# Kernel tuning notes

Measured on AMD Instinct MI355X. Metric: run time of the kernel, lower is better.

Reference implementation:

```python
import jax, jax.numpy as jnp
import numpy as np

T = 2048         # seq_len (nbatch in original code)
IN = 384         # input_size (npts)
H = 2 * IN       # hidden_dim = 768
NL = 10          # n_layers
NOUT = 384       # output_size


def setup_inputs() -> dict:
    key = jax.random.key(0)
    ks = jax.random.split(key, 12)
    s_in = 1.0 / np.sqrt(H)  # PyTorch GRU init scale
    inp = {
        "x": jax.random.normal(ks[0], (T, IN), dtype=jnp.float32),
        # layer 0 (input_size -> H)
        "w_ih0": jax.random.uniform(ks[1], (3 * H, IN), jnp.float32, -s_in, s_in),
        "w_hh0": jax.random.uniform(ks[2], (3 * H, H), jnp.float32, -s_in, s_in),
        "b_ih0": jax.random.uniform(ks[3], (3 * H,), jnp.float32, -s_in, s_in),
        "b_hh0": jax.random.uniform(ks[4], (3 * H,), jnp.float32, -s_in, s_in),
        # layers 1..9 (H -> H), stacked
        "w_ih": jax.random.uniform(ks[5], (NL - 1, 3 * H, H), jnp.float32, -s_in, s_in),
        "w_hh": jax.random.uniform(ks[6], (NL - 1, 3 * H, H), jnp.float32, -s_in, s_in),
        "b_ih": jax.random.uniform(ks[7], (NL - 1, 3 * H), jnp.float32, -s_in, s_in),
        "b_hh": jax.random.uniform(ks[8], (NL - 1, 3 * H), jnp.float32, -s_in, s_in),
        # final linear head
        "fc_w": jax.random.uniform(ks[9], (NOUT, H), jnp.float32, -s_in, s_in),
        "fc_b": jax.random.uniform(ks[10], (NOUT,), jnp.float32, -s_in, s_in),
    }
    return inp


def _gru_layer(xs, w_ih, w_hh, b_ih, b_hh):
    # xs: [T, D_in] -> ys: [T, H]. PyTorch GRU cell semantics.
    gi = xs @ w_ih.T + b_ih          # [T, 3H] input projections, batched GEMM up front

    def step(h, gi_t):
        gh = h @ w_hh.T + b_hh       # [3H]
        i_r, i_z, i_n = jnp.split(gi_t, 3)
        h_r, h_z, h_n = jnp.split(gh, 3)
        r = jax.nn.sigmoid(i_r + h_r)
        z = jax.nn.sigmoid(i_z + h_z)
        n = jnp.tanh(i_n + r * h_n)
        h_new = (1.0 - z) * n + z * h
        return h_new, h_new

    h0 = jnp.zeros((xs.shape[1] if False else w_hh.shape[1],), xs.dtype)  # [H]
    _, ys = jax.lax.scan(step, h0, gi)
    return ys


def reference(x, w_ih0, w_hh0, b_ih0, b_hh0, w_ih, w_hh, b_ih, b_hh, fc_w, fc_b):
    # batch_size = 1 in the original; hidden initialized to zeros each call.
    h = _gru_layer(x, w_ih0, w_hh0, b_ih0, b_hh0)   # layer 0
    for l in range(NL - 1):                           # layers 1..9 (fixed small loop)
        h = _gru_layer(h, w_ih[l], w_hh[l], b_ih[l], b_hh[l])
    out = h @ fc_w.T + fc_b                           # [T, NOUT]
    return out
```

## Files before the change

### kernel.cpp

```cpp
#include <hip/hip_runtime.h>


#define T_SEQ 2048
#define H_DIM 768
#define IN0   384
#define G3    2304
#define NLAYER 10
#define BPL   24
#define NBLK  (NLAYER * BPL)
#define UPB   32
#define NTHR  512
#define NOUT  384
#define CTR_STRIDE 32
#define RING  16
#define WPR   384
#define WIH_STRIDE 776
#define HCS_STRIDE 52
#define HSD_STRIDE 56
#define HSD0_STRIDE 32

typedef _Float16 half2_t __attribute__((ext_vector_type(2)));
typedef _Float16 half8_t __attribute__((ext_vector_type(8)));
typedef unsigned long long u64;

__device__ __forceinline__ float sigm(float x) { return 1.0f / (1.0f + __expf(-x)); }

__device__ __forceinline__ u64 ld64(const u64* p) {
    return __hip_atomic_load(p, __ATOMIC_RELAXED, __HIP_MEMORY_SCOPE_AGENT);
}
__device__ __forceinline__ void st64(u64* p, u64 v) {
    __hip_atomic_store(p, v, __ATOMIC_RELAXED, __HIP_MEMORY_SCOPE_AGENT);
}
__device__ __forceinline__ unsigned ldctr(const unsigned* p) {
    return __hip_atomic_load(p, __ATOMIC_RELAXED, __HIP_MEMORY_SCOPE_AGENT);
}
__device__ __forceinline__ int tagok(u64 v, unsigned tg) {
    return (((unsigned)v & 31u) == tg) & ((((unsigned)(v >> 32)) & 31u) == tg);
}

__device__ __forceinline__ float dot8(half8_t h, half8_t w, float acc) {
    union U { half8_t v; unsigned u[4]; };
    U H; H.v = h; U W; W.v = w;
#pragma unroll
    for (int j = 0; j < 4; ++j) {
#if __has_builtin(__builtin_amdgcn_fdot2)
        acc = __builtin_amdgcn_fdot2(__builtin_bit_cast(half2_t, H.u[j]),
                                     __builtin_bit_cast(half2_t, W.u[j]), acc, false);
#else
        half2_t a = __builtin_bit_cast(half2_t, H.u[j]);
        half2_t b = __builtin_bit_cast(half2_t, W.u[j]);
        asm volatile("v_dot2_f32_f16 %0, %1, %2, %0" : "+v"(acc) : "v"(a), "v"(b));
#endif
    }
    return acc;
}

extern "C" __global__ __launch_bounds__(NTHR, 1) void gru_flow(
    const float* __restrict__ x,
    const float* __restrict__ wih0,
    const float* __restrict__ whh0,
    const float* __restrict__ bih0,
    const float* __restrict__ bhh0,
    const float* __restrict__ wihS,
    const float* __restrict__ whhS,
    const float* __restrict__ bihS,
    const float* __restrict__ bhhS,
    u64* __restrict__ ring64,
    float* __restrict__ h9,
    unsigned int* __restrict__ ctr)
{
    __shared__ __align__(16) _Float16 wih16[96 * WIH_STRIDE];
    __shared__ __align__(16) float    hcs[2][16 * HCS_STRIDE];
    __shared__ __align__(16) _Float16 hsd16[2][16 * HSD_STRIDE];

    const int tid  = threadIdx.x;
    const int lane = tid & 63;
    const int wv   = tid >> 6;
    const int p    = lane & 15;
    const int ulocal = wv * 4 + (lane >> 4);
    const int bid  = blockIdx.x;
    const int layer = bid / BPL;
    const int sub   = bid % BPL;
    const int uglob = sub * UPB + ulocal;
    const int Din   = layer ? H_DIM : IN0;

    const float* wihL = layer ? wihS + (size_t)(layer - 1) * G3 * H_DIM : wih0;
    const float* whhL = layer ? whhS + (size_t)(layer - 1) * G3 * H_DIM : whh0;
    const float* bihL = layer ? bihS + (size_t)(layer - 1) * G3 : bih0;
    const float* bhhL = layer ? bhhS + (size_t)(layer - 1) * G3 : bhh0;

    float4 wr[3][12];
#pragma unroll
    for (int gate = 0; gate < 3; ++gate) {
        const float4* src = (const float4*)(whhL + (size_t)(uglob + gate * H_DIM) * H_DIM + 48 * p);
#pragma unroll
        for (int i = 0; i < 12; ++i) wr[gate][i] = src[i];
    }
    const float bhr  = bhhL[uglob], bhz = bhhL[uglob + H_DIM], bhn  = bhhL[uglob + 2 * H_DIM];
    const float bir  = bihL[uglob], biz = bihL[uglob + H_DIM], bin_ = bihL[uglob + 2 * H_DIM];

    for (int rr = 0; rr < 12; ++rr) {
        const int r = wv * 12 + rr;
        const int u = r / 3, G = r % 3;
        const float* src = wihL + (size_t)(sub * UPB + u + G * H_DIM) * Din;
        _Float16* dst = wih16 + r * WIH_STRIDE;
        for (int k = lane; k < Din; k += 64) dst[k] = (_Float16)src[k];
    }
    __syncthreads();

    auto stage_hsd = [&](int b, int w, u64 v) {
        const int s = w / 24, idx = (2 * w) % 48;
        const _Float16 a = (_Float16)__uint_as_float((unsigned)v & ~31u);
        const _Float16 c = (_Float16)__uint_as_float((unsigned)(v >> 32) & ~31u);
        const unsigned pk = (unsigned)__builtin_bit_cast(unsigned short, a)
                          | ((unsigned)__builtin_bit_cast(unsigned short, c) << 16);
        *(unsigned*)&hsd16[b][s * HSD_STRIDE + idx] = pk;
    };

    float gi_r = 0.f, gi_z = 0.f, gi_n = 0.f;
    auto ih_gemv = [&](int b) {
        float sr = 0.f, sz = 0.f, sn = 0.f;
        if (layer) {
            const half8_t* h8 = (const half8_t*)(&hsd16[b][p * HSD_STRIDE]);
            const half8_t* w0 = (const half8_t*)(wih16 + (ulocal * 3 + 0) * WIH_STRIDE + 48 * p);
            const half8_t* w1 = (const half8_t*)(wih16 + (ulocal * 3 + 1) * WIH_STRIDE + 48 * p);
            const half8_t* wn = (const half8_t*)(wih16 + (ulocal * 3 + 2) * WIH_STRIDE + 48 * p);
#pragma unroll
            for (int i = 0; i < 6; ++i) {
                const half8_t hv = h8[i];
                sr = dot8(hv, w0[i], sr);
                sz = dot8(hv, w1[i], sz);
                sn = dot8(hv, wn[i], sn);
            }
        } else {
            const half8_t* h8 = (const half8_t*)(&hsd16[b][p * HSD0_STRIDE]);
            const half8_t* w0 = (const half8_t*)(wih16 + (ulocal * 3 + 0) * WIH_STRIDE + 24 * p);
            const half8_t* w1 = (const half8_t*)(wih16 + (ulocal * 3 + 1) * WIH_STRIDE + 24 * p);
            const half8_t* wn = (const half8_t*)(wih16 + (ulocal * 3 + 2) * WIH_STRIDE + 24 * p);
#pragma unroll
            for (int i = 0; i < 3; ++i) {
                const half8_t hv = h8[i];
                sr = dot8(hv, w0[i], sr);
                sz = dot8(hv, w1[i], sz);
                sn = dot8(hv, wn[i], sn);
            }
        }
#pragma unroll
        for (int off = 1; off <= 8; off <<= 1) {
            sr += __shfl_xor(sr, off, 64);
            sz += __shfl_xor(sz, off, 64);
            sn += __shfl_xor(sn, off, 64);
        }
        gi_r = sr + bir; gi_z = sz + biz; gi_n = sn + bin_;
    };

    if (layer) {
        if (tid < WPR) {
            const u64* sp = ring64 + (size_t)(layer - 1) * RING * WPR;
            u64 v = 0;
            while (!tagok(v, 1u)) v = ld64(sp + tid);
            stage_hsd(1, tid, v);
        }
    } else {
        if (tid < IN0) hsd16[1][(tid / 24) * HSD0_STRIDE + tid % 24] = (_Float16)x[tid];
    }
    __syncthreads();
    ih_gemv(1);

    u64 ca0 = 0, sa0 = 0;
    float xs = 0.f;
    if (tid < WPR) {
        if (layer) sa0 = ld64(ring64 + ((size_t)(layer - 1) * RING + 1) * WPR + tid);
        else       xs  = x[IN0 + tid];
    }

    unsigned bp = 0;

    for (int t = 0; t < T_SEQ; ++t) {
        const int b = t & 1;
        const bool have_s = (t + 1) < T_SEQ;

        if (layer != NLAYER - 1 && t >= 16 && (t & 3) == 0) {
            const unsigned tgt = 24u * (unsigned)((t - 12) >> 2);
            while (bp < tgt) {
                __builtin_amdgcn_s_sleep(2);
                bp = ldctr(&ctr[(layer + 1) * CTR_STRIDE]);
            }
        }

        if (t > 0 && tid < WPR) {
            const u64* hr = ring64 + ((size_t)layer * RING + ((t - 1) & (RING - 1))) * WPR;
            const unsigned tg = (unsigned)t & 31u;
            u64 v = ca0;
            while (!tagok(v, tg)) v = ld64(hr + tid);
            const int s = tid / 24, idx = (2 * tid) % 48;
            float2 hv;
            hv.x = __uint_as_float((unsigned)v & ~31u);
            hv.y = __uint_as_float((unsigned)(v >> 32) & ~31u);
            *(float2*)&hcs[b][s * HCS_STRIDE + idx] = hv;
        }

        if (have_s) {
            if (layer) {
                if (tid < WPR) {
                    const u64* sp = ring64 + ((size_t)(layer - 1) * RING + ((t + 1) & (RING - 1))) * WPR;
                    const unsigned tg2 = (unsigned)(t + 2) & 31u;
                    u64 v = sa0;
                    while (!tagok(v, tg2)) v = ld64(sp + tid);
                    stage_hsd(b, tid, v);
                }
            } else {
                if (tid < IN0) hsd16[b][(tid / 24) * HSD0_STRIDE + tid % 24] = (_Float16)xs;
            }
        }

        __syncthreads();

        float ar = 0.f, az = 0.f, an = 0.f;
        if (t > 0) {
            const float4* hs = (const float4*)(&hcs[b][p * HCS_STRIDE]);
#pragma unroll
            for (int i = 0; i < 12; ++i) {
                const float4 h4 = hs[i];
                ar += h4.x * wr[0][i].x + h4.y * wr[0][i].y + h4.z * wr[0][i].z + h4.w * wr[0][i].w;
                az += h4.x * wr[1][i].x + h4.y * wr[1][i].y + h4.z * wr[1][i].z + h4.w * wr[1][i].w;
                an += h4.x * wr[2][i].x + h4.y * wr[2][i].y + h4.z * wr[2][i].z + h4.w * wr[2][i].w;
            }
        }
#pragma unroll
        for (int off = 1; off <= 8; off <<= 1) {
            ar += __shfl_xor(ar, off, 64);
            az += __shfl_xor(az, off, 64);
            an += __shfl_xor(an, off, 64);
        }
        {
            const float hp = (t > 0) ? hcs[b][(uglob / 48) * HCS_STRIDE + uglob % 48] : 0.f;
            const float r = sigm(ar + bhr + gi_r);
            const float z = sigm(az + bhz + gi_z);
            const float n = tanhf(gi_n + r * (an + bhn));
            const float hnew = (1.f - z) * n + z * hp;
            const float hpart = __shfl_xor(hnew, 16, 64);
            if (p == 0 && (lane & 16) == 0) {
                const unsigned tg1 = (unsigned)(t + 1) & 31u;
                const unsigned lo = (__float_as_uint(hnew)  & ~31u) | tg1;
                const unsigned hi = (__float_as_uint(hpart) & ~31u) | tg1;
                st64(&ring64[((size_t)layer * RING + (t & (RING - 1))) * WPR + (uglob >> 1)],
                     ((u64)hi << 32) | (u64)lo);
            }
            if (layer == NLAYER - 1 && p == 0) h9[(size_t)t * H_DIM + uglob] = hnew;
        }

        if (have_s && tid < WPR) {
            ca0 = ld64(ring64 + ((size_t)layer * RING + (t & (RING - 1))) * WPR + tid);
            if ((t + 2) < T_SEQ) {
                if (layer) sa0 = ld64(ring64 + ((size_t)(layer - 1) * RING + ((t + 2) & (RING - 1))) * WPR + tid);
                else       xs  = x[(size_t)(t + 2) * IN0 + tid];
            }
        }

        if (have_s) ih_gemv(b);

        if ((t & 3) == 3) {
            if (tid == 0 && layer)
                __hip_atomic_fetch_add(&ctr[layer * CTR_STRIDE], 1u,
                                       __ATOMIC_RELAXED, __HIP_MEMORY_SCOPE_AGENT);
            if (layer != NLAYER - 1)
                bp = ldctr(&ctr[(layer + 1) * CTR_STRIDE]);
        }
    }
}

extern "C" __global__ __launch_bounds__(NOUT, 1) void fc_head(
    const float* __restrict__ h,
    const float* __restrict__ fw,
    const float* __restrict__ fb,
    float* __restrict__ out)
{
    __shared__ float hs[H_DIM];
    const int t = blockIdx.x;
    const float* hr = h + (size_t)t * H_DIM;
    for (int k = threadIdx.x; k < H_DIM; k += NOUT) hs[k] = hr[k];
    __syncthreads();

    const int o = threadIdx.x;
    const float4* wr4 = (const float4*)(fw + (size_t)o * H_DIM);
    const float4* hs4 = (const float4*)hs;
    float acc = fb[o];
#pragma unroll 8
    for (int k = 0; k < H_DIM / 4; ++k) {
        const float4 w = wr4[k], hv = hs4[k];
        acc += w.x * hv.x + w.y * hv.y + w.z * hv.z + w.w * hv.w;
    }
    out[(size_t)t * NOUT + o] = acc;
}

extern "C" void kernel_launch(void* const* d_in, const int* in_sizes, int n_in,
                              void* d_out, int out_size, void* d_ws, size_t ws_size,
                              hipStream_t stream)
{
    const float* x    = (const float*)d_in[0];
    const float* wih0 = (const float*)d_in[1];
    const float* whh0 = (const float*)d_in[2];
    const float* bih0 = (const float*)d_in[3];
    const float* bhh0 = (const float*)d_in[4];
    const float* wihS = (const float*)d_in[5];
    const float* whhS = (const float*)d_in[6];
    const float* bihS = (const float*)d_in[7];
    const float* bhhS = (const float*)d_in[8];
    const float* fcw  = (const float*)d_in[9];
    const float* fcb  = (const float*)d_in[10];

    char* ws = (char*)d_ws;
    unsigned int* ctr = (unsigned int*)ws;
    u64* ring64 = (u64*)(ws + 65536);
    float* h9   = (float*)(ws + 65536 + (size_t)NLAYER * RING * WPR * 8);

    hipMemsetAsync(ctr, 0, 65536, stream);
    hipMemsetAsync(ring64, 0, (size_t)NLAYER * RING * WPR * 8, stream);

    hipLaunchKernelGGL(gru_flow, dim3(NBLK), dim3(NTHR), 0, stream,
                       x, wih0, whh0, bih0, bhh0, wihS, whhS, bihS, bhhS,
                       ring64, h9, ctr);

    hipLaunchKernelGGL(fc_head, dim3(T_SEQ), dim3(NOUT), 0, stream,
                       h9, fcw, fcb, (float*)d_out);
}
```

Measured before the change: 7.046 ms.

## Split GRU stack into two 5-layer phases with XCD-local role assignment

Instead of one persistent kernel running all 10 layers as a dataflow pipeline, the work is split into two launches of 5 layers each, joined by an fp16 intermediate buffer. Each block reads its XCD id and claims a layer role on that XCD, so all blocks of a layer sit on one XCD and can exchange the recurrent hidden state through near-scope (sc0) loads and stores. A second ring carries state downstream to the next layer over agent scope. The goal is lower latency on the per-step recurrent sync. In exchange the pipeline fill is paid twice, role claiming adds spin waits at startup, and results depend on how the hardware places blocks on XCDs.

```diff
diff --git a/kernel.cpp b/kernel.cpp
--- a/kernel.cpp
+++ b/kernel.cpp
@@ -5,9 +5,10 @@
 #define H_DIM 768
 #define IN0   384
 #define G3    2304
-#define NLAYER 10
+#define NLL   5
 #define BPL   24
-#define NBLK  (NLAYER * BPL)
+#define NROLE (NLL * BPL)
+#define NBLK  256
 #define UPB   32
 #define NTHR  512
 #define NOUT  384
@@ -25,11 +26,20 @@
 
 __device__ __forceinline__ float sigm(float x) { return 1.0f / (1.0f + __expf(-x)); }
 
-__device__ __forceinline__ u64 ld64(const u64* p) {
+__device__ __forceinline__ u64 ld64_far(const u64* p) {
     return __hip_atomic_load(p, __ATOMIC_RELAXED, __HIP_MEMORY_SCOPE_AGENT);
 }
-__device__ __forceinline__ void st64(u64* p, u64 v) {
+__device__ __forceinline__ void st64_far(u64* p, u64 v) {
     __hip_atomic_store(p, v, __ATOMIC_RELAXED, __HIP_MEMORY_SCOPE_AGENT);
+}
+__device__ __forceinline__ u64 ld64_near(const u64* p) {
+    u64 v;
+    asm volatile("global_load_dwordx2 %0, %1, off sc0\n\ts_waitcnt vmcnt(0)"
+                 : "=v"(v) : "v"(p) : "memory");
+    return v;
+}
+__device__ __forceinline__ void st64_near(u64* p, u64 v) {
+    asm volatile("global_store_dwordx2 %0, %1, off sc0" :: "v"(p), "v"(v) : "memory");
 }
 __device__ __forceinline__ unsigned ldctr(const unsigned* p) {
     return __hip_atomic_load(p, __ATOMIC_RELAXED, __HIP_MEMORY_SCOPE_AGENT);
@@ -55,39 +65,74 @@
     return acc;
 }
 
-extern "C" __global__ __launch_bounds__(NTHR, 1) void gru_flow(
-    const float* __restrict__ x,
-    const float* __restrict__ wih0,
-    const float* __restrict__ whh0,
-    const float* __restrict__ bih0,
-    const float* __restrict__ bhh0,
-    const float* __restrict__ wihS,
-    const float* __restrict__ whhS,
-    const float* __restrict__ bihS,
-    const float* __restrict__ bhhS,
-    u64* __restrict__ ring64,
-    float* __restrict__ h9,
-    unsigned int* __restrict__ ctr)
+extern "C" __global__ __launch_bounds__(NTHR, 1) void gru_phase(
+    const void* fin, int fin_is16, int layer_base,
+    const float* __restrict__ wih0, const float* __restrict__ whh0,
+    const float* __restrict__ bih0, const float* __restrict__ bhh0,
+    const float* __restrict__ wihS, const float* __restrict__ whhS,
+    const float* __restrict__ bihS, const float* __restrict__ bhhS,
+    u64* __restrict__ ring_loc, u64* __restrict__ ring_dwn,
+    unsigned int* __restrict__ ctr, int* __restrict__ taken,
+    int* __restrict__ rolexcd,
+    float* __restrict__ hout32, _Float16* __restrict__ hout16)
 {
     __shared__ __align__(16) _Float16 wih16[96 * WIH_STRIDE];
     __shared__ __align__(16) float    hcs[2][16 * HCS_STRIDE];
     __shared__ __align__(16) _Float16 hsd16[2][16 * HSD_STRIDE];
+    __shared__ int s_role, s_local;
 
     const int tid  = threadIdx.x;
     const int lane = tid & 63;
     const int wv   = tid >> 6;
     const int p    = lane & 15;
     const int ulocal = wv * 4 + (lane >> 4);
-    const int bid  = blockIdx.x;
-    const int layer = bid / BPL;
-    const int sub   = bid % BPL;
+
+    if (tid == 0) {
+        int xcd = 0;
+        asm volatile("s_getreg_b32 %0, hwreg(20, 0, 32)" : "=s"(xcd));
+        xcd &= 7;
+        int role = -1;
+        if (xcd < NLL) {
+            const int b0 = xcd * BPL;
+            for (int r = b0; r < b0 + BPL; ++r)
+                if (atomicExch(&taken[r], 1) == 0) { role = r; break; }
+        }
+        if (role < 0) {
+            for (int w = 0; w < 300; ++w) __builtin_amdgcn_s_sleep(8);
+            for (int r = 0; r < NROLE && role < 0; ++r)
+                if (atomicExch(&taken[r], 1) == 0) role = r;
+        }
+        int loc = 0;
+        if (role >= 0) {
+            __hip_atomic_store(&rolexcd[role], xcd + 1,
+                               __ATOMIC_RELEASE, __HIP_MEMORY_SCOPE_AGENT);
+            const int lb = (role / BPL) * BPL;
+            loc = 1;
+            for (int r = lb; r < lb + BPL; ++r) {
+                int v;
+                while ((v = __hip_atomic_load(&rolexcd[r], __ATOMIC_ACQUIRE,
+                                              __HIP_MEMORY_SCOPE_AGENT)) == 0)
+                    __builtin_amdgcn_s_sleep(2);
+                if (v != xcd + 1) loc = 0;
+            }
+        }
+        s_role = role; s_local = loc;
+    }
+    __syncthreads();
+    const int role = s_role;
+    if (role < 0) return;
+    const bool uselocal = (s_local != 0);
+    const int layer = role / BPL;
+    const int sub   = role % BPL;
     const int uglob = sub * UPB + ulocal;
-    const int Din   = layer ? H_DIM : IN0;
-
-    const float* wihL = layer ? wihS + (size_t)(layer - 1) * G3 * H_DIM : wih0;
-    const float* whhL = layer ? whhS + (size_t)(layer - 1) * G3 * H_DIM : whh0;
-    const float* bihL = layer ? bihS + (size_t)(layer - 1) * G3 : bih0;
-    const float* bhhL = layer ? bhhS + (size_t)(layer - 1) * G3 : bhh0;
+    const int lg    = layer_base + layer;
+    const int Din   = lg ? H_DIM : IN0;
+    const bool din384 = (Din == IN0);
+
+    const float* wihL = lg ? wihS + (size_t)(lg - 1) * G3 * H_DIM : wih0;
+    const float* whhL = lg ? whhS + (size_t)(lg - 1) * G3 * H_DIM : whh0;
+    const float* bihL = lg ? bihS + (size_t)(lg - 1) * G3 : bih0;
+    const float* bhhL = lg ? bhhS + (size_t)(lg - 1) * G3 : bhh0;
 
     float4 wr[3][12];
 #pragma unroll
@@ -116,11 +161,23 @@
                           | ((unsigned)__builtin_bit_cast(unsigned short, c) << 16);
         *(unsigned*)&hsd16[b][s * HSD_STRIDE + idx] = pk;
     };
+    auto stage_fin = [&](int b, int row) {
+        if (din384) {
+            if (tid < IN0)
+                hsd16[b][(tid / 24) * HSD0_STRIDE + tid % 24] = fin_is16
+                    ? ((const _Float16*)fin)[(size_t)row * IN0 + tid]
+                    : (_Float16)((const float*)fin)[(size_t)row * IN0 + tid];
+        } else {
+            const _Float16* f16 = (const _Float16*)fin;
+            for (int vi = tid; vi < H_DIM; vi += NTHR)
+                hsd16[b][(vi / 48) * HSD_STRIDE + vi % 48] = f16[(size_t)row * H_DIM + vi];
+        }
+    };
 
     float gi_r = 0.f, gi_z = 0.f, gi_n = 0.f;
     auto ih_gemv = [&](int b) {
         float sr = 0.f, sz = 0.f, sn = 0.f;
-        if (layer) {
+        if (!din384) {
             const half8_t* h8 = (const half8_t*)(&hsd16[b][p * HSD_STRIDE]);
             const half8_t* w0 = (const half8_t*)(wih16 + (ulocal * 3 + 0) * WIH_STRIDE + 48 * p);
             const half8_t* w1 = (const half8_t*)(wih16 + (ulocal * 3 + 1) * WIH_STRIDE + 48 * p);
@@ -128,9 +185,7 @@
 #pragma unroll
             for (int i = 0; i < 6; ++i) {
                 const half8_t hv = h8[i];
-                sr = dot8(hv, w0[i], sr);
-                sz = dot8(hv, w1[i], sz);
-                sn = dot8(hv, wn[i], sn);
+                sr = dot8(hv, w0[i], sr); sz = dot8(hv, w1[i], sz); sn = dot8(hv, wn[i], sn);
             }
         } else {
             const half8_t* h8 = (const half8_t*)(&hsd16[b][p * HSD0_STRIDE]);
@@ -140,9 +195,7 @@
 #pragma unroll
             for (int i = 0; i < 3; ++i) {
                 const half8_t hv = h8[i];
-                sr = dot8(hv, w0[i], sr);
-                sz = dot8(hv, w1[i], sz);
-                sn = dot8(hv, wn[i], sn);
+                sr = dot8(hv, w0[i], sr); sz = dot8(hv, w1[i], sz); sn = dot8(hv, wn[i], sn);
             }
         }
 #pragma unroll
@@ -156,23 +209,20 @@
 
     if (layer) {
         if (tid < WPR) {
-            const u64* sp = ring64 + (size_t)(layer - 1) * RING * WPR;
+            const u64* sp = ring_dwn + (size_t)(layer - 1) * RING * WPR + tid;
             u64 v = 0;
-            while (!tagok(v, 1u)) v = ld64(sp + tid);
+            while (!tagok(v, 1u)) v = ld64_far(sp);
             stage_hsd(1, tid, v);
         }
     } else {
-        if (tid < IN0) hsd16[1][(tid / 24) * HSD0_STRIDE + tid % 24] = (_Float16)x[tid];
+        stage_fin(1, 0);
     }
     __syncthreads();
     ih_gemv(1);
 
-    u64 ca0 = 0, sa0 = 0;
-    float xs = 0.f;
-    if (tid < WPR) {
-        if (layer) sa0 = ld64(ring64 + ((size_t)(layer - 1) * RING + 1) * WPR + tid);
-        else       xs  = x[IN0 + tid];
-    }
+    u64 sa0 = 0;
+    if (layer && tid < WPR)
+        sa0 = ld64_far(ring_dwn + ((size_t)(layer - 1) * RING + 1) * WPR + tid);
 
     unsigned bp = 0;
 
@@ -180,7 +230,7 @@
         const int b = t & 1;
         const bool have_s = (t + 1) < T_SEQ;
 
-        if (layer != NLAYER - 1 && t >= 16 && (t & 3) == 0) {
+        if (layer != NLL - 1 && t >= 16 && (t & 3) == 0) {
             const unsigned tgt = 24u * (unsigned)((t - 12) >> 2);
             while (bp < tgt) {
                 __builtin_amdgcn_s_sleep(2);
@@ -189,10 +239,11 @@
         }
 
         if (t > 0 && tid < WPR) {
-            const u64* hr = ring64 + ((size_t)layer * RING + ((t - 1) & (RING - 1))) * WPR;
+            const u64* hr = ring_loc + ((size_t)layer * RING + ((t - 1) & (RING - 1))) * WPR + tid;
             const unsigned tg = (unsigned)t & 31u;
-            u64 v = ca0;
-            while (!tagok(v, tg)) v = ld64(hr + tid);
+            u64 v = ld64_near(hr);
+            int k = 0;
+            while (!tagok(v, tg)) v = (++k & 1) ? ld64_far(hr) : ld64_near(hr);
             const int s = tid / 24, idx = (2 * tid) % 48;
             float2 hv;
             hv.x = __uint_as_float((unsigned)v & ~31u);
@@ -203,14 +254,14 @@
         if (have_s) {
             if (layer) {
                 if (tid < WPR) {
-                    const u64* sp = ring64 + ((size_t)(layer - 1) * RING + ((t + 1) & (RING - 1))) * WPR;
+                    const u64* sp = ring_dwn + ((size_t)(layer - 1) * RING + ((t + 1) & (RING - 1))) * WPR + tid;
                     const unsigned tg2 = (unsigned)(t + 2) & 31u;
                     u64 v = sa0;
-                    while (!tagok(v, tg2)) v = ld64(sp + tid);
+                    while (!tagok(v, tg2)) v = ld64_far(sp);
                     stage_hsd(b, tid, v);
                 }
             } else {
-                if (tid < IN0) hsd16[b][(tid / 24) * HSD0_STRIDE + tid % 24] = (_Float16)xs;
+                stage_fin(b, t + 1);
             }
         }
 
@@ -244,19 +295,20 @@
                 const unsigned tg1 = (unsigned)(t + 1) & 31u;
                 const unsigned lo = (__float_as_uint(hnew)  & ~31u) | tg1;
                 const unsigned hi = (__float_as_uint(hpart) & ~31u) | tg1;
-                st64(&ring64[((size_t)layer * RING + (t & (RING - 1))) * WPR + (uglob >> 1)],
-                     ((u64)hi << 32) | (u64)lo);
-            }
-            if (layer == NLAYER - 1 && p == 0) h9[(size_t)t * H_DIM + uglob] = hnew;
-        }
-
-        if (have_s && tid < WPR) {
-            ca0 = ld64(ring64 + ((size_t)layer * RING + (t & (RING - 1))) * WPR + tid);
-            if ((t + 2) < T_SEQ) {
-                if (layer) sa0 = ld64(ring64 + ((size_t)(layer - 1) * RING + ((t + 2) & (RING - 1))) * WPR + tid);
-                else       xs  = x[(size_t)(t + 2) * IN0 + tid];
-            }
-        }
+                const u64 w = ((u64)hi << 32) | (u64)lo;
+                const size_t base = ((size_t)layer * RING + (t & (RING - 1))) * WPR + (uglob >> 1);
+                if (uselocal) st64_near(&ring_loc[base], w);
+                else          st64_far (&ring_loc[base], w);
+                if (layer < NLL - 1) st64_far(&ring_dwn[base], w);
+            }
+            if (layer == NLL - 1 && p == 0) {
+                if (hout16) hout16[(size_t)t * H_DIM + uglob] = (_Float16)hnew;
+                else        hout32[(size_t)t * H_DIM + uglob] = hnew;
+            }
+        }
+
+        if (layer && tid < WPR && (t + 2) < T_SEQ)
+            sa0 = ld64_far(ring_dwn + ((size_t)(layer - 1) * RING + ((t + 2) & (RING - 1))) * WPR + tid);
 
         if (have_s) ih_gemv(b);
 
@@ -264,7 +316,7 @@
             if (tid == 0 && layer)
                 __hip_atomic_fetch_add(&ctr[layer * CTR_STRIDE], 1u,
                                        __ATOMIC_RELAXED, __HIP_MEMORY_SCOPE_AGENT);
-            if (layer != NLAYER - 1)
+            if (layer != NLL - 1)
                 bp = ldctr(&ctr[(layer + 1) * CTR_STRIDE]);
         }
     }
@@ -311,16 +363,34 @@
     const float* fcb  = (const float*)d_in[10];
 
     char* ws = (char*)d_ws;
-    unsigned int* ctr = (unsigned int*)ws;
-    u64* ring64 = (u64*)(ws + 65536);
-    float* h9   = (float*)(ws + 65536 + (size_t)NLAYER * RING * WPR * 8);
-
-    hipMemsetAsync(ctr, 0, 65536, stream);
-    hipMemsetAsync(ring64, 0, (size_t)NLAYER * RING * WPR * 8, stream);
-
-    hipLaunchKernelGGL(gru_flow, dim3(NBLK), dim3(NTHR), 0, stream,
-                       x, wih0, whh0, bih0, bhh0, wihS, whhS, bihS, bhhS,
-                       ring64, h9, ctr);
+    const size_t RSZ = (size_t)NLL * RING * WPR * 8;
+    int*      taken0   = (int*)(ws + 0);
+    int*      taken1   = (int*)(ws + 1024);
+    int*      rolexcd0 = (int*)(ws + 2048);
+    int*      rolexcd1 = (int*)(ws + 3072);
+    unsigned* ctr0     = (unsigned*)(ws + 8192);
+    unsigned* ctr1     = (unsigned*)(ws + 16384);
+    u64* ring_loc0 = (u64*)(ws + 65536);
+    u64* ring_dwn0 = (u64*)(ws + 65536 + RSZ);
+    u64* ring_loc1 = (u64*)(ws + 65536 + 2 * RSZ);
+    u64* ring_dwn1 = (u64*)(ws + 65536 + 3 * RSZ);
+    _Float16* h4 = (_Float16*)(ws + 1048576);
+    float*    h9 = (float*)(ws + 4194304);
+
+    hipMemsetAsync(ws, 0, 65536, stream);
+    hipMemsetAsync(ws + 65536, 0, 4 * RSZ, stream);
+
+    hipLaunchKernelGGL(gru_phase, dim3(NBLK), dim3(NTHR), 0, stream,
+                       (const void*)x, 0, 0,
+                       wih0, whh0, bih0, bhh0, wihS, whhS, bihS, bhhS,
+                       ring_loc0, ring_dwn0, ctr0, taken0, rolexcd0,
+                       (float*)nullptr, h4);
+
+    hipLaunchKernelGGL(gru_phase, dim3(NBLK), dim3(NTHR), 0, stream,
+                       (const void*)h4, 1, NLL,
+                       wih0, whh0, bih0, bhh0, wihS, whhS, bihS, bhhS,
+                       ring_loc1, ring_dwn1, ctr1, taken1, rolexcd1,
+                       h9, (_Float16*)nullptr);
 
     hipLaunchKernelGGL(fc_head, dim3(T_SEQ), dim3(NOUT), 0, stream,
                        h9, fcw, fcb, (float*)d_out);
```

After: 10.65 ms. 51.2% more time.
